# Kernel optimization log

Hardware: AMD Instinct MI355X
Metric: run time of the kernel (lower is better)

## Reference

```python
import jax, jax.numpy as jnp
import numpy as np

N_NODES = 50000
N_EDGES = 1_600_000
D_IN = 128
D_HID = 128
D_OUT = 128


def _linear_init(key, out_dim, in_dim, bias=True):
    k1, k2 = jax.random.split(key)
    bound = 1.0 / np.sqrt(in_dim)
    W = jax.random.uniform(k1, (out_dim, in_dim), jnp.float32, -bound, bound)
    if bias:
        b = jax.random.uniform(k2, (out_dim,), jnp.float32, -bound, bound)
        return W, b
    return W, None


def _leconv_params(key, in_dim, out_dim):
    k1, k2, k3 = jax.random.split(key, 3)
    W1, b1 = _linear_init(k1, out_dim, in_dim, bias=True)   # lin1 (applied to x_j)
    W2, _ = _linear_init(k2, out_dim, in_dim, bias=False)   # lin2 (applied to x_i)
    W3, b3 = _linear_init(k3, out_dim, in_dim, bias=True)   # lin3 (skip on x_i)
    return W1, b1, W2, W3, b3


def setup_inputs() -> dict:
    key = jax.random.key(0)
    kx, ke, kw, k_in, k_mid, k_out = jax.random.split(key, 6)
    x = jax.random.normal(kx, (N_NODES, D_IN), jnp.float32)
    edge_index = jax.random.randint(ke, (2, N_EDGES), 0, N_NODES, dtype=jnp.int32)
    edge_weight = jax.random.uniform(kw, (N_EDGES,), jnp.float32)
    iW1, ib1, iW2, iW3, ib3 = _leconv_params(k_in, D_IN, D_HID)
    mW1, mb1, mW2, mW3, mb3 = _leconv_params(k_mid, D_HID, D_HID)
    oW1, ob1, oW2, oW3, ob3 = _leconv_params(k_out, D_HID, D_OUT)
    return {
        "x": x, "edge_index": edge_index, "edge_weight": edge_weight,
        "in_W1": iW1, "in_b1": ib1, "in_W2": iW2, "in_W3": iW3, "in_b3": ib3,
        "mid_W1": mW1, "mid_b1": mb1, "mid_W2": mW2, "mid_W3": mW3, "mid_b3": mb3,
        "out_W1": oW1, "out_b1": ob1, "out_W2": oW2, "out_W3": oW3, "out_b3": ob3,
        "number_of_layers": 4,
    }


def _leconv(h, src, dst, ew, W1, b1, W2, W3, b3):
    # out_i = sum_{j->i} e_ji * ((W1 x_j + b1) - W2 x_i) + (W3 x_i + b3)
    a = h @ W1.T + b1          # [N, F_out]
    b = h @ W2.T               # [N, F_out]
    msg = ew[:, None] * (a[src] - b[dst])              # [E, F_out]
    agg = jax.ops.segment_sum(msg, dst, num_segments=h.shape[0])
    return agg + h @ W3.T + b3


def _lrelu(x):
    return jnp.where(x >= 0, x, 0.1 * x)


def reference(x, edge_index, edge_weight,
              in_W1, in_b1, in_W2, in_W3, in_b3,
              mid_W1, mid_b1, mid_W2, mid_W3, mid_b3,
              out_W1, out_b1, out_W2, out_W3, out_b3,
              number_of_layers):
    src, dst = edge_index[0], edge_index[1]
    h = _lrelu(_leconv(x, src, dst, edge_weight, in_W1, in_b1, in_W2, in_W3, in_b3))
    for _ in range(number_of_layers - 2):  # shared inner weights, as in the torch module
        h = _lrelu(_leconv(h, src, dst, edge_weight, mid_W1, mid_b1, mid_W2, mid_W3, mid_b3))
    h = _lrelu(_leconv(h, src, dst, edge_weight, out_W1, out_b1, out_W2, out_W3, out_b3))
    return jax.nn.sigmoid(h)
```

## Files before the change

### kernel.cpp

```cpp
#include <hip/hip_runtime.h>
#include <hip/hip_fp16.h>
#include <math.h>

#define D 128
#define CSH 13
#define BSH 9
#define NB_MAX 128

typedef _Float16 f16;
typedef __attribute__((ext_vector_type(8))) _Float16 f16x8;
typedef __attribute__((ext_vector_type(4))) float f32x4;


__global__ __launch_bounds__(256) void binA_count(
    const int* __restrict__ dst, int* __restrict__ bucketCount, int E)
{
    __shared__ int hist[NB_MAX];
    int tid = threadIdx.x;
    if (tid < NB_MAX) hist[tid] = 0;
    __syncthreads();
    int base = blockIdx.x * 4096;
    for (int i = tid; i < 4096; i += 256) {
        int e = base + i;
        if (e < E) atomicAdd(&hist[dst[e] >> BSH], 1);
    }
    __syncthreads();
    if (tid < NB_MAX && hist[tid]) atomicAdd(&bucketCount[tid], hist[tid]);
}

__global__ void bucket_scan(
    const int* __restrict__ bucketCount, int* __restrict__ bucketBase,
    int* __restrict__ bucketCursor, int* __restrict__ row_off,
    int NBUC, int E, int N)
{
    if (threadIdx.x == 0 && blockIdx.x == 0) {
        int p = 0;
        for (int b = 0; b < NBUC; ++b) {
            bucketBase[b] = p; bucketCursor[b] = p; p += bucketCount[b];
        }
        bucketBase[NBUC] = p;
        row_off[N] = E;
    }
}

__global__ __launch_bounds__(256) void binA_scatter(
    const int* __restrict__ src, const int* __restrict__ dst,
    const float* __restrict__ ew, int* __restrict__ bucketCursor,
    int4* __restrict__ binned, int E)
{
    __shared__ int hist[NB_MAX], off[NB_MAX], cbase[NB_MAX];
    int tid = threadIdx.x;
    if (tid < NB_MAX) { hist[tid] = 0; off[tid] = 0; }
    __syncthreads();
    int base = blockIdx.x * 4096;
    for (int i = tid; i < 4096; i += 256) {
        int e = base + i;
        if (e < E) atomicAdd(&hist[dst[e] >> BSH], 1);
    }
    __syncthreads();
    if (tid < NB_MAX && hist[tid])
        cbase[tid] = atomicAdd(&bucketCursor[tid], hist[tid]);
    __syncthreads();
    for (int i = tid; i < 4096; i += 256) {
        int e = base + i;
        if (e < E) {
            int d = dst[e];
            int b = d >> BSH;
            int pos = cbase[b] + atomicAdd(&off[b], 1);
            binned[pos] = make_int4(src[e], __float_as_int(ew[e]), d, 0);
        }
    }
}

__global__ __launch_bounds__(1024) void binB_kernel(
    const int4* __restrict__ binned, const int* __restrict__ bucketBase,
    int2* __restrict__ edge_s, int* __restrict__ row_off,
    float* __restrict__ sdeg, int N, int nchunk)
{
    __shared__ int hist[4096];
    __shared__ int cur[4096];
    __shared__ float sdl[512];
    __shared__ int wsum[16];

    int b    = blockIdx.x;
    int tid  = threadIdx.x;
    int ebeg = bucketBase[b], eend = bucketBase[b + 1];
    int node0 = b << BSH;
    int nib   = min(512, N - node0);

    for (int i = tid; i < 4096; i += 1024) hist[i] = 0;
    for (int i = tid; i < 512; i += 1024) sdl[i] = 0.f;
    __syncthreads();

    for (int e = ebeg + tid; e < eend; e += 1024) {
        int4 ed = binned[e];
        int dl = ed.z - node0;
        int ch = ((unsigned)ed.x) >> CSH;
        atomicAdd(&hist[dl * nchunk + ch], 1);
        atomicAdd(&sdl[dl], __int_as_float(ed.y));
    }
    __syncthreads();

    int t4 = tid * 4;
    int h0 = hist[t4], h1 = hist[t4 + 1], h2 = hist[t4 + 2], h3 = hist[t4 + 3];
    int sum = h0 + h1 + h2 + h3;
    int lane = tid & 63, wid = tid >> 6;
    int x = sum;
    #pragma unroll
    for (int o = 1; o < 64; o <<= 1) { int t = __shfl_up(x, o); if (lane >= o) x += t; }
    if (lane == 63) wsum[wid] = x;
    __syncthreads();
    if (tid < 16) {
        int y = wsum[tid];
        #pragma unroll
        for (int o = 1; o < 16; o <<= 1) { int t = __shfl_up(y, o, 16); if (tid >= o) y += t; }
        wsum[tid] = y;
    }
    __syncthreads();
    int excl = (wid ? wsum[wid - 1] : 0) + x - sum;
    cur[t4] = excl; cur[t4 + 1] = excl + h0;
    cur[t4 + 2] = excl + h0 + h1; cur[t4 + 3] = excl + h0 + h1 + h2;
    __syncthreads();

    for (int dl = tid; dl < nib; dl += 1024) {
        row_off[node0 + dl] = ebeg + cur[dl * nchunk];
        sdeg[node0 + dl]    = sdl[dl];
    }
    __syncthreads();

    for (int e = ebeg + tid; e < eend; e += 1024) {
        int4 ed = binned[e];
        int dl = ed.z - node0;
        int ch = ((unsigned)ed.x) >> CSH;
        int pos = ebeg + atomicAdd(&cur[dl * nchunk + ch], 1);
        edge_s[pos] = make_int2(ed.x, ed.y);
    }
}

__global__ __launch_bounds__(256) void pack_kernel(
    const float* __restrict__ W1, const float* __restrict__ W2,
    const float* __restrict__ W3, f16* __restrict__ Wp)
{
    int idx = blockIdx.x * 256 + threadIdx.x;
    if (idx >= 6144) return;
    int lane = idx & 63;
    int t    = idx >> 6;
    int ks   = t & 3;
    int mot  = t >> 2;
    int m    = mot >> 3;
    int ot   = mot & 7;
    const float* W = (m == 0) ? W1 : (m == 1) ? W2 : W3;
    int o  = ot * 16 + (lane & 15);
    int kb = ks * 32 + (lane >> 4) * 8;
    f16x8 hi, lo;
    #pragma unroll
    for (int j = 0; j < 8; ++j) {
        float v = W[(size_t)o * D + kb + j];
        f16 hh = (f16)v;
        hi[j] = hh;
        lo[j] = (f16)(v - (float)hh);
    }
    size_t base = (size_t)ks * 24576 + (size_t)mot * 1024 + (size_t)lane * 8;
    *(f16x8*)&Wp[base]       = hi;
    *(f16x8*)&Wp[base + 512] = lo;
}


__global__ __launch_bounds__(256, 2) void gemm_kernel(
    const float* __restrict__ in, const f16* __restrict__ Wp,
    const float* __restrict__ b1, const float* __restrict__ b3,
    const float* __restrict__ sdeg, float* __restrict__ aA,
    float* __restrict__ aB, float* __restrict__ base_out,
    int N, int ntiles, int gridb)
{
    int tid  = threadIdx.x;
    int lane = tid & 63;
    int wid  = tid >> 6;
    int col  = lane & 15;
    int g    = lane >> 4;

    f16x8 w[3][2][4][2];
    #pragma unroll
    for (int m = 0; m < 3; ++m)
        #pragma unroll
        for (int oti = 0; oti < 2; ++oti) {
            int mot = m * 8 + wid * 2 + oti;
            #pragma unroll
            for (int ks = 0; ks < 4; ++ks) {
                const f16* p = Wp + (size_t)ks * 24576 + (size_t)mot * 1024 + (size_t)lane * 8;
                w[m][oti][ks][0] = *(const f16x8*)p;
                w[m][oti][ks][1] = *(const f16x8*)(p + 512);
            }
        }

    float bi1[2], bi3[2];
    #pragma unroll
    for (int oti = 0; oti < 2; ++oti) {
        int o = (wid * 2 + oti) * 16 + col;
        bi1[oti] = b1[o];
        bi3[oti] = b3[o];
    }

    for (int t = blockIdx.x; t < ntiles; t += gridb) {
        int n0   = t * 16;
        int nrow = n0 + col;

        f32x4 acc[3][2];
        #pragma unroll
        for (int m = 0; m < 3; ++m)
            #pragma unroll
            for (int oti = 0; oti < 2; ++oti)
                acc[m][oti] = (f32x4){0.f, 0.f, 0.f, 0.f};

        #pragma unroll
        for (int ks = 0; ks < 4; ++ks) {
            float av[8];
            if (nrow < N) {
                float4 a0 = *(const float4*)&in[(size_t)nrow * D + ks * 32 + g * 8];
                float4 a1 = *(const float4*)&in[(size_t)nrow * D + ks * 32 + g * 8 + 4];
                av[0] = a0.x; av[1] = a0.y; av[2] = a0.z; av[3] = a0.w;
                av[4] = a1.x; av[5] = a1.y; av[6] = a1.z; av[7] = a1.w;
            } else {
                #pragma unroll
                for (int j = 0; j < 8; ++j) av[j] = 0.f;
            }
            f16x8 ahi, alo;
            #pragma unroll
            for (int j = 0; j < 8; ++j) {
                f16 hh = (f16)av[j];
                ahi[j] = hh;
                alo[j] = (f16)(av[j] - (float)hh);
            }
            #pragma unroll
            for (int m = 0; m < 3; ++m)
                #pragma unroll
                for (int oti = 0; oti < 2; ++oti) {
                    acc[m][oti] = __builtin_amdgcn_mfma_f32_16x16x32_f16(ahi, w[m][oti][ks][0], acc[m][oti], 0, 0, 0);
                    acc[m][oti] = __builtin_amdgcn_mfma_f32_16x16x32_f16(alo, w[m][oti][ks][0], acc[m][oti], 0, 0, 0);
                    acc[m][oti] = __builtin_amdgcn_mfma_f32_16x16x32_f16(ahi, w[m][oti][ks][1], acc[m][oti], 0, 0, 0);
                }
        }

        float* ah = (wid < 2) ? aA : aB;
        #pragma unroll
        for (int oti = 0; oti < 2; ++oti) {
            int o  = (wid * 2 + oti) * 16 + col;
            int oh = o & 63;
            #pragma unroll
            for (int r = 0; r < 4; ++r) {
                int node = n0 + g * 4 + r;
                if (node < N) {
                    float sv   = sdeg[node];
                    float aval = acc[0][oti][r] + bi1[oti];
                    float bval = acc[2][oti][r] + bi3[oti] - sv * acc[1][oti][r];
                    ah[(size_t)node * 64 + oh]     = aval;
                    base_out[(size_t)node * D + o] = bval;
                }
            }
        }
    }
}


__global__ __launch_bounds__(256) void agg_kernel(
    const float* __restrict__ aA, const float* __restrict__ aB,
    const float* __restrict__ base, const int* __restrict__ row_off,
    const int2* __restrict__ edge_s, float* __restrict__ out, int N, int last)
{
    int lane = threadIdx.x & 63;
    int wid  = threadIdx.x >> 6;
    int node = blockIdx.x * 2 + (wid >> 1);
    int half = wid & 1;
    if (node >= N) return;
    const float* aH = half ? aB : aA;
    int hofs = half << 6;

    float acc = base[(size_t)node * D + hofs + lane];
    int beg = row_off[node];
    int end = row_off[node + 1];

    int e = beg;
    if ((e & 1) && e < end) {
        int2 ed = edge_s[e];
        acc = fmaf(__int_as_float(ed.y), aH[(size_t)ed.x * 64 + lane], acc);
        ++e;
    }
    for (; e + 16 <= end; e += 16) {
        int4 ed[8];
        #pragma unroll
        for (int i = 0; i < 8; ++i) ed[i] = *(const int4*)&edge_s[e + i * 2];
        float v[16];
        #pragma unroll
        for (int i = 0; i < 8; ++i) {
            v[2 * i]     = aH[(size_t)ed[i].x * 64 + lane];
            v[2 * i + 1] = aH[(size_t)ed[i].z * 64 + lane];
        }
        #pragma unroll
        for (int i = 0; i < 8; ++i) {
            acc = fmaf(__int_as_float(ed[i].y), v[2 * i], acc);
            acc = fmaf(__int_as_float(ed[i].w), v[2 * i + 1], acc);
        }
    }
    for (; e + 4 <= end; e += 4) {
        int4 e0 = *(const int4*)&edge_s[e];
        int4 e1 = *(const int4*)&edge_s[e + 2];
        float v0 = aH[(size_t)e0.x * 64 + lane];
        float v1 = aH[(size_t)e0.z * 64 + lane];
        float v2 = aH[(size_t)e1.x * 64 + lane];
        float v3 = aH[(size_t)e1.z * 64 + lane];
        acc = fmaf(__int_as_float(e0.y), v0, acc);
        acc = fmaf(__int_as_float(e0.w), v1, acc);
        acc = fmaf(__int_as_float(e1.y), v2, acc);
        acc = fmaf(__int_as_float(e1.w), v3, acc);
    }
    for (; e < end; ++e) {
        int2 ed = edge_s[e];
        acc = fmaf(__int_as_float(ed.y), aH[(size_t)ed.x * 64 + lane], acc);
    }

    acc = acc >= 0.f ? acc : 0.1f * acc;
    if (last) acc = 1.f / (1.f + __expf(-acc));
    out[(size_t)node * D + hofs + lane] = acc;
}


extern "C" void kernel_launch(void* const* d_in, const int* in_sizes, int n_in,
                              void* d_out, int out_size, void* d_ws, size_t ws_size,
                              hipStream_t stream) {
    const float* x   = (const float*)d_in[0];
    const int*   ei  = (const int*)d_in[1];
    const float* ew  = (const float*)d_in[2];
    const float* iW1 = (const float*)d_in[3];
    const float* ib1 = (const float*)d_in[4];
    const float* iW2 = (const float*)d_in[5];
    const float* iW3 = (const float*)d_in[6];
    const float* ib3 = (const float*)d_in[7];
    const float* mW1 = (const float*)d_in[8];
    const float* mb1 = (const float*)d_in[9];
    const float* mW2 = (const float*)d_in[10];
    const float* mW3 = (const float*)d_in[11];
    const float* mb3 = (const float*)d_in[12];
    const float* oW1 = (const float*)d_in[13];
    const float* ob1 = (const float*)d_in[14];
    const float* oW2 = (const float*)d_in[15];
    const float* oW3 = (const float*)d_in[16];
    const float* ob3 = (const float*)d_in[17];

    int N = in_sizes[0] / D;
    int E = in_sizes[2];
    const int* src = ei;
    const int* dst = ei + E;
    int nchunk = (N + (1 << CSH) - 1) >> CSH;
    int NBUC   = (N + (1 << BSH) - 1) >> BSH;

    char* wsp = (char*)d_ws;
    size_t off = 0;
    auto alloc = [&](size_t bytes) -> void* {
        void* p = wsp + off;
        off += (bytes + 255) & ~(size_t)255;
        return p;
    };
    float* h        = (float*)alloc((size_t)N * D * 4);
    float* base     = (float*)alloc((size_t)N * D * 4);
    float* aA       = (float*)alloc((size_t)N * 64 * 4);
    float* aB       = (float*)alloc((size_t)N * 64 * 4);
    float* sdeg     = (float*)alloc((size_t)N * 4);
    int*   row_off  = (int*)alloc((size_t)(N + 1) * 4);
    int2*  edge_s   = (int2*)alloc((size_t)E * 8);
    int*   bucketCount  = (int*)alloc((size_t)(NBUC + 1) * 4);
    int*   bucketBase   = (int*)alloc((size_t)(NBUC + 1) * 4);
    int*   bucketCursor = (int*)alloc((size_t)(NBUC + 1) * 4);
    f16*   Wp       = (f16*)alloc((size_t)3 * 98304 * 2);

    int4* binned = (int4*)h;

    hipMemsetAsync(bucketCount, 0, (size_t)(NBUC + 1) * 4, stream);

    int aggblocks = (N + 1) / 2;
    int ntiles    = (N + 15) / 16;
    int gridb     = 512;
    int abblocks  = (E + 4095) / 4096;

    pack_kernel<<<24, 256, 0, stream>>>(iW1, iW2, iW3, Wp);
    pack_kernel<<<24, 256, 0, stream>>>(mW1, mW2, mW3, Wp + 98304);
    pack_kernel<<<24, 256, 0, stream>>>(oW1, oW2, oW3, Wp + 2 * 98304);

    binA_count<<<abblocks, 256, 0, stream>>>(dst, bucketCount, E);
    bucket_scan<<<1, 64, 0, stream>>>(bucketCount, bucketBase, bucketCursor,
                                      row_off, NBUC, E, N);
    binA_scatter<<<abblocks, 256, 0, stream>>>(src, dst, ew, bucketCursor,
                                               binned, E);
    binB_kernel<<<NBUC, 1024, 0, stream>>>(binned, bucketBase, edge_s,
                                           row_off, sdeg, N, nchunk);

    gemm_kernel<<<gridb, 256, 0, stream>>>(x, Wp, ib1, ib3, sdeg, aA, aB, base, N, ntiles, gridb);
    agg_kernel<<<aggblocks, 256, 0, stream>>>(aA, aB, base, row_off, edge_s, h, N, 0);
    for (int l = 0; l < 2; ++l) {
        gemm_kernel<<<gridb, 256, 0, stream>>>(h, Wp + 98304, mb1, mb3, sdeg, aA, aB, base, N, ntiles, gridb);
        agg_kernel<<<aggblocks, 256, 0, stream>>>(aA, aB, base, row_off, edge_s, h, N, 0);
    }
    gemm_kernel<<<gridb, 256, 0, stream>>>(h, Wp + 2 * 98304, ob1, ob3, sdeg, aA, aB, base, N, ntiles, gridb);
    agg_kernel<<<aggblocks, 256, 0, stream>>>(aA, aB, base, row_off, edge_s, (float*)d_out, N, 1);
}
```

Measured before the change: 679.9 us.

## Split aggregation into per-half passes to keep gather table cache-resident

Each aggregation now runs as two launches, one per 64-column half of the feature table (aA, then aB). Each launch gathers from a single 12.8 MB table, which is meant to improve L2/MALL hit rates for the random neighbour reads. Edge-list and base loads and output stores become nontemporal so they do not evict the gather table. The main loop unroll grows from 16 to 24 edges and launch bounds request occupancy 3. The cost is that the edge list is read twice per layer and there are extra kernel launches.

```diff
diff --git a/kernel.cpp b/kernel.cpp
--- a/kernel.cpp
+++ b/kernel.cpp
@@ -10,6 +10,7 @@
 typedef _Float16 f16;
 typedef __attribute__((ext_vector_type(8))) _Float16 f16x8;
 typedef __attribute__((ext_vector_type(4))) float f32x4;
+typedef __attribute__((ext_vector_type(4))) int i32x4;
 
 
 __global__ __launch_bounds__(256) void binA_count(
@@ -262,20 +263,16 @@
 }
 
 
-__global__ __launch_bounds__(256) void agg_kernel(
-    const float* __restrict__ aA, const float* __restrict__ aB,
-    const float* __restrict__ base, const int* __restrict__ row_off,
-    const int2* __restrict__ edge_s, float* __restrict__ out, int N, int last)
+__global__ __launch_bounds__(256, 3) void agg_kernel(
+    const float* __restrict__ aH, const float* __restrict__ base,
+    const int* __restrict__ row_off, const int2* __restrict__ edge_s,
+    float* __restrict__ out, int N, int hofs, int last)
 {
     int lane = threadIdx.x & 63;
-    int wid  = threadIdx.x >> 6;
-    int node = blockIdx.x * 2 + (wid >> 1);
-    int half = wid & 1;
+    int node = blockIdx.x * 4 + (threadIdx.x >> 6);
     if (node >= N) return;
-    const float* aH = half ? aB : aA;
-    int hofs = half << 6;
-
-    float acc = base[(size_t)node * D + hofs + lane];
+
+    float acc = __builtin_nontemporal_load(&base[(size_t)node * D + hofs + lane]);
     int beg = row_off[node];
     int end = row_off[node + 1];
 
@@ -285,33 +282,39 @@
         acc = fmaf(__int_as_float(ed.y), aH[(size_t)ed.x * 64 + lane], acc);
         ++e;
     }
-    for (; e + 16 <= end; e += 16) {
-        int4 ed[8];
-        #pragma unroll
-        for (int i = 0; i < 8; ++i) ed[i] = *(const int4*)&edge_s[e + i * 2];
-        float v[16];
-        #pragma unroll
-        for (int i = 0; i < 8; ++i) {
+    for (; e + 24 <= end; e += 24) {
+        i32x4 ed[12];
+        #pragma unroll
+        for (int i = 0; i < 12; ++i)
+            ed[i] = __builtin_nontemporal_load((const i32x4*)&edge_s[e + i * 2]);
+        float v[24];
+        #pragma unroll
+        for (int i = 0; i < 12; ++i) {
             v[2 * i]     = aH[(size_t)ed[i].x * 64 + lane];
             v[2 * i + 1] = aH[(size_t)ed[i].z * 64 + lane];
         }
         #pragma unroll
-        for (int i = 0; i < 8; ++i) {
+        for (int i = 0; i < 12; ++i) {
             acc = fmaf(__int_as_float(ed[i].y), v[2 * i], acc);
             acc = fmaf(__int_as_float(ed[i].w), v[2 * i + 1], acc);
         }
     }
-    for (; e + 4 <= end; e += 4) {
-        int4 e0 = *(const int4*)&edge_s[e];
-        int4 e1 = *(const int4*)&edge_s[e + 2];
-        float v0 = aH[(size_t)e0.x * 64 + lane];
-        float v1 = aH[(size_t)e0.z * 64 + lane];
-        float v2 = aH[(size_t)e1.x * 64 + lane];
-        float v3 = aH[(size_t)e1.z * 64 + lane];
-        acc = fmaf(__int_as_float(e0.y), v0, acc);
-        acc = fmaf(__int_as_float(e0.w), v1, acc);
-        acc = fmaf(__int_as_float(e1.y), v2, acc);
-        acc = fmaf(__int_as_float(e1.w), v3, acc);
+    for (; e + 8 <= end; e += 8) {
+        i32x4 ed[4];
+        #pragma unroll
+        for (int i = 0; i < 4; ++i)
+            ed[i] = __builtin_nontemporal_load((const i32x4*)&edge_s[e + i * 2]);
+        float v[8];
+        #pragma unroll
+        for (int i = 0; i < 4; ++i) {
+            v[2 * i]     = aH[(size_t)ed[i].x * 64 + lane];
+            v[2 * i + 1] = aH[(size_t)ed[i].z * 64 + lane];
+        }
+        #pragma unroll
+        for (int i = 0; i < 4; ++i) {
+            acc = fmaf(__int_as_float(ed[i].y), v[2 * i], acc);
+            acc = fmaf(__int_as_float(ed[i].w), v[2 * i + 1], acc);
+        }
     }
     for (; e < end; ++e) {
         int2 ed = edge_s[e];
@@ -320,7 +323,7 @@
 
     acc = acc >= 0.f ? acc : 0.1f * acc;
     if (last) acc = 1.f / (1.f + __expf(-acc));
-    out[(size_t)node * D + hofs + lane] = acc;
+    __builtin_nontemporal_store(acc, &out[(size_t)node * D + hofs + lane]);
 }
 
 
@@ -376,10 +379,10 @@
 
     hipMemsetAsync(bucketCount, 0, (size_t)(NBUC + 1) * 4, stream);
 
-    int aggblocks = (N + 1) / 2;
-    int ntiles    = (N + 15) / 16;
-    int gridb     = 512;
-    int abblocks  = (E + 4095) / 4096;
+    int ablocks  = (N + 3) / 4;
+    int ntiles   = (N + 15) / 16;
+    int gridb    = 512;
+    int abblocks = (E + 4095) / 4096;
 
     pack_kernel<<<24, 256, 0, stream>>>(iW1, iW2, iW3, Wp);
     pack_kernel<<<24, 256, 0, stream>>>(mW1, mW2, mW3, Wp + 98304);
@@ -394,11 +397,14 @@
                                            row_off, sdeg, N, nchunk);
 
     gemm_kernel<<<gridb, 256, 0, stream>>>(x, Wp, ib1, ib3, sdeg, aA, aB, base, N, ntiles, gridb);
-    agg_kernel<<<aggblocks, 256, 0, stream>>>(aA, aB, base, row_off, edge_s, h, N, 0);
+    agg_kernel<<<ablocks, 256, 0, stream>>>(aA, base, row_off, edge_s, h, N, 0, 0);
+    agg_kernel<<<ablocks, 256, 0, stream>>>(aB, base, row_off, edge_s, h, N, 64, 0);
     for (int l = 0; l < 2; ++l) {
         gemm_kernel<<<gridb, 256, 0, stream>>>(h, Wp + 98304, mb1, mb3, sdeg, aA, aB, base, N, ntiles, gridb);
-        agg_kernel<<<aggblocks, 256, 0, stream>>>(aA, aB, base, row_off, edge_s, h, N, 0);
+        agg_kernel<<<ablocks, 256, 0, stream>>>(aA, base, row_off, edge_s, h, N, 0, 0);
+        agg_kernel<<<ablocks, 256, 0, stream>>>(aB, base, row_off, edge_s, h, N, 64, 0);
     }
     gemm_kernel<<<gridb, 256, 0, stream>>>(h, Wp + 2 * 98304, ob1, ob3, sdeg, aA, aB, base, N, ntiles, gridb);
-    agg_kernel<<<aggblocks, 256, 0, stream>>>(aA, aB, base, row_off, edge_s, (float*)d_out, N, 1);
-}
+    agg_kernel<<<ablocks, 256, 0, stream>>>(aA, base, row_off, edge_s, (float*)d_out, N, 0, 1);
+    agg_kernel<<<ablocks, 256, 0, stream>>>(aB, base, row_off, edge_s, (float*)d_out, N, 64, 1);
+}
```

Result: slower. 771.3 us (+13.5%).
